# Kernel tuning notes

Hardware: AMD Instinct MI355X
Metric: run time of the kernel (lower is better)

Reference implementation:

```python
import jax, jax.numpy as jnp
import numpy as np

B, S, D, H = 2, 2048, 2048, 16
HD = D // H  # 128


def setup_inputs() -> dict:
    key = jax.random.key(0)
    ks = jax.random.split(key, 5)
    x = jax.random.normal(ks[0], (B, S, D), dtype=jnp.float32)
    scale = 1.0 / np.sqrt(D)
    wq = jax.random.normal(ks[1], (D, D), dtype=jnp.float32) * scale
    wk = jax.random.normal(ks[2], (D, D), dtype=jnp.float32) * scale
    wv = jax.random.normal(ks[3], (D, D), dtype=jnp.float32) * scale
    wo = jax.random.normal(ks[4], (D, D), dtype=jnp.float32) * scale
    # RoPE frequencies: theta = 10000, freqs_cis[t, j] = exp(i * t / theta^(2j/HD))
    inv_freq = 1.0 / (10000.0 ** (jnp.arange(0, HD, 2, dtype=jnp.float32) / HD))  # [HD/2]
    t = jnp.arange(S, dtype=jnp.float32)
    ang = jnp.outer(t, inv_freq)  # [S, HD/2]
    freqs_cos = jnp.cos(ang)
    freqs_sin = jnp.sin(ang)
    # Additive causal mask [S, S]
    neg = jnp.float32(-1e9)
    mask = jnp.triu(jnp.full((S, S), neg, dtype=jnp.float32), k=1)
    return {"x": x, "wq": wq, "wk": wk, "wv": wv, "wo": wo,
            "freqs_cos": freqs_cos, "freqs_sin": freqs_sin,
            "mask": mask, "start_pos": 0}


def _rope(t, cos, sin):
    # t: [B, S, H, HD]; cos/sin: [S, HD/2] broadcast as [1, S, 1, HD/2]
    tr = t.reshape(t.shape[:-1] + (HD // 2, 2))
    xr, xi = tr[..., 0], tr[..., 1]
    c = cos[None, :, None, :]
    s = sin[None, :, None, :]
    out_r = xr * c - xi * s
    out_i = xr * s + xi * c
    return jnp.stack([out_r, out_i], axis=-1).reshape(t.shape)


def reference(x, wq, wk, wv, wo, freqs_cos, freqs_sin, mask, start_pos):
    bsz, seqlen, _ = x.shape
    # nn.Linear: y = x @ W.T
    xq = jnp.einsum('bsd,ed->bse', x, wq).reshape(bsz, seqlen, H, HD)
    xk = jnp.einsum('bsd,ed->bse', x, wk).reshape(bsz, seqlen, H, HD)
    xv = jnp.einsum('bsd,ed->bse', x, wv).reshape(bsz, seqlen, H, HD)
    xq = _rope(xq, freqs_cos, freqs_sin)
    xk = _rope(xk, freqs_cos, freqs_sin)
    # [B, H, S, HD]
    xq = xq.transpose(0, 2, 1, 3)
    xk = xk.transpose(0, 2, 1, 3)
    xv = xv.transpose(0, 2, 1, 3)
    scores = jnp.einsum('bhqd,bhkd->bhqk', xq, xk) / jnp.sqrt(jnp.float32(HD))
    scores = scores + mask[None, None, :, :]
    probs = jax.nn.softmax(scores.astype(jnp.float32), axis=-1).astype(xq.dtype)
    out = jnp.einsum('bhqk,bhkd->bhqd', probs, xv)
    out = out.transpose(0, 2, 1, 3).reshape(bsz, seqlen, H * HD)
    return jnp.einsum('bse,de->bsd', out, wo)
```

## Files before the change

### kernel.cpp

```cpp
#include <hip/hip_runtime.h>


#define SQ 2048
#define DQ 2048
#define HQ 16
#define HDQ 128

typedef short bf16x8 __attribute__((ext_vector_type(8)));
typedef short bf16x4 __attribute__((ext_vector_type(4)));
typedef float f32x4 __attribute__((ext_vector_type(4)));

#define WAITVM4 asm volatile("s_waitcnt vmcnt(4)" ::: "memory")
#define WAITVM3 asm volatile("s_waitcnt vmcnt(3)" ::: "memory")
#define WAITVM2 asm volatile("s_waitcnt vmcnt(2)" ::: "memory")
#define WAITVM0 asm volatile("s_waitcnt vmcnt(0)" ::: "memory")

__device__ __forceinline__ short f2bf(float f) {
  union { float f; unsigned u; } v; v.f = f;
  unsigned r = (v.u + 0x7FFFu + ((v.u >> 16) & 1u)) >> 16;
  return (short)r;
}
__device__ __forceinline__ float bf2f(short b) {
  union { unsigned u; float f; } v; v.u = ((unsigned)(unsigned short)b) << 16;
  return v.f;
}
__device__ __forceinline__ void gload_lds16(const void* g, void* l) {
  __builtin_amdgcn_global_load_lds(
      (const __attribute__((address_space(1))) void*)g,
      (__attribute__((address_space(3))) void*)l, 16, 0, 0);
}

__global__ void cvt5_kernel(const float* __restrict__ x, const float* __restrict__ wq,
                            const float* __restrict__ wk, const float* __restrict__ wv,
                            const float* __restrict__ wo, short* __restrict__ xb,
                            short* __restrict__ wqb, short* __restrict__ wkb,
                            short* __restrict__ wvb, short* __restrict__ wob) {
  int bi = blockIdx.x;
  const float* src;
  short* dst;
  int off;
  if (bi < 4096) {
    src = x; dst = xb; off = bi;
  } else {
    int t = bi - 4096, wsel = t >> 11;
    off = t & 2047;
    src = (wsel == 0) ? wq : (wsel == 1) ? wk : (wsel == 2) ? wv : wo;
    dst = (wsel == 0) ? wqb : (wsel == 1) ? wkb : (wsel == 2) ? wvb : wob;
  }
  int i = off * 256 + threadIdx.x;
  const f32x4* p = (const f32x4*)src + (size_t)i * 2;
  f32x4 a = p[0], b = p[1];
  bf16x8 o;
  o[0] = f2bf(a[0]); o[1] = f2bf(a[1]); o[2] = f2bf(a[2]); o[3] = f2bf(a[3]);
  o[4] = f2bf(b[0]); o[5] = f2bf(b[1]); o[6] = f2bf(b[2]); o[7] = f2bf(b[3]);
  *((bf16x8*)dst + i) = o;
}

__global__ void tpose_kernel(const float* __restrict__ fc, const float* __restrict__ fs,
                             float* __restrict__ fct, float* __restrict__ fst) {
  __shared__ float tile[64][65];
  int s0 = blockIdx.x * 64, t = threadIdx.x;
#pragma unroll
  for (int it = 0; it < 16; ++it) {
    int idx = it * 256 + t;
    int r = idx >> 6, ii = idx & 63;
    tile[r][ii] = fc[(size_t)(s0 + r) * 64 + ii];
  }
  __syncthreads();
#pragma unroll
  for (int it = 0; it < 16; ++it) {
    int idx = it * 256 + t;
    int ii = idx >> 6, so = idx & 63;
    fct[(size_t)ii * 2048 + s0 + so] = tile[so][ii];
  }
  __syncthreads();
#pragma unroll
  for (int it = 0; it < 16; ++it) {
    int idx = it * 256 + t;
    int r = idx >> 6, ii = idx & 63;
    tile[r][ii] = fs[(size_t)(s0 + r) * 64 + ii];
  }
  __syncthreads();
#pragma unroll
  for (int it = 0; it < 16; ++it) {
    int idx = it * 256 + t;
    int ii = idx >> 6, so = idx & 63;
    fst[(size_t)ii * 2048 + s0 + so] = tile[so][ii];
  }
}

template <int BN, int MODE>
__global__ __launch_bounds__(512, 4) void gemmT(const short* __restrict__ A,
                                                const short* __restrict__ W,
                                                short* __restrict__ oQ, short* __restrict__ oK,
                                                short* __restrict__ oV, float* __restrict__ oF,
                                                const float* __restrict__ cosTt,
                                                const float* __restrict__ sinTt) {
  constexpr int NFR = BN / 64;
  constexpr int NIB = BN / 16;
  __shared__ __align__(16) short As[3][128 * 32];
  __shared__ __align__(16) short Bs[3][BN * 32];
  const int K = DQ;
  const int NT = K / 32;
  int x = blockIdx.x, xcd = x & 7, l = x >> 3;
  int by, bx;
  if (MODE == 0) {
    int xr = xcd >> 2, xc = xcd & 3;
    by = xr * 16 + (l >> 3);
    bx = xc * 8 + (l & 7);
  } else {
    int xr = xcd >> 1, xc = xcd & 1;
    by = xr * 8 + (l >> 3);
    bx = xc * 8 + (l & 7);
  }
  int m0 = by * 128, n0 = bx * BN;
  int tid = threadIdx.x, wid = tid >> 6, lane = tid & 63;
  int wr = wid >> 2, wc = wid & 3;
  f32x4 acc[4][NFR] = {};

  auto stageA = [&](int kt, int buf) {
    int g = wid * 64 + lane;
    int r = g >> 2, q = g & 3;
    gload_lds16(A + (size_t)(m0 + r) * K + kt * 32 + ((q ^ (((r >> 3) & 1) << 1)) * 8),
                &As[buf][wid * 512]);
  };
  auto stageB = [&](int kt, int buf) {
#pragma unroll
    for (int i = wid; i < NIB; i += 8) {
      int g = i * 64 + lane;
      int r = g >> 2, q = g & 3;
      gload_lds16(W + (size_t)(n0 + r) * K + kt * 32 + ((q ^ (((r >> 3) & 1) << 1)) * 8),
                  &Bs[buf][i * 512]);
    }
  };

  stageA(0, 0); stageB(0, 0);
  stageA(1, 1); stageB(1, 1);
  if (BN == 192 && wid < 4) { WAITVM3; } else { WAITVM2; }
  __builtin_amdgcn_s_barrier();

  int cc = (lane >> 4) * 8;
  int cur = 0, nbuf = 2;
#pragma unroll 1
  for (int t = 0; t < NT; ++t) {
    bool st = (t + 2) < NT;
    bf16x8 bfr[NFR], af[4];
#pragma unroll
    for (int nf = 0; nf < NFR; ++nf) {
      int br = wc * (BN / 4) + nf * 16 + (lane & 15);
      bfr[nf] = *(const bf16x8*)&Bs[cur][br * 32 + (cc ^ (((br >> 3) & 1) << 4))];
    }
#pragma unroll
    for (int i = 0; i < 4; ++i) {
      int fr = wr * 64 + i * 16 + (lane & 15);
      af[i] = *(const bf16x8*)&As[cur][fr * 32 + (cc ^ (((fr >> 3) & 1) << 4))];
    }
    if (st) { stageA(t + 2, nbuf); stageB(t + 2, nbuf); }
    __builtin_amdgcn_s_setprio(1);
#pragma unroll
    for (int i = 0; i < 4; ++i)
#pragma unroll
      for (int nf = 0; nf < NFR; ++nf)
        acc[i][nf] = __builtin_amdgcn_mfma_f32_16x16x32_bf16(af[i], bfr[nf], acc[i][nf], 0, 0, 0);
    __builtin_amdgcn_s_setprio(0);
    if (st) {
      if (BN == 192 && wid < 4) { WAITVM3; } else { WAITVM2; }
    } else {
      WAITVM0;
    }
    __builtin_amdgcn_s_barrier();
    cur = (cur == 2) ? 0 : cur + 1;
    nbuf = (nbuf == 2) ? 0 : nbuf + 1;
  }
  if (MODE == 1) {
#pragma unroll
    for (int mf = 0; mf < 4; ++mf) {
      int mb = m0 + wr * 64 + mf * 16 + (lane >> 4) * 4;
#pragma unroll
      for (int nf = 0; nf < NFR; ++nf) {
        int n_lin = n0 + wc * (BN / 4) + nf * 16 + (lane & 15);
#pragma unroll
        for (int j = 0; j < 4; ++j)
          oF[(size_t)(mb + j) * DQ + n_lin] = acc[mf][nf][j];
      }
    }
  } else {
#pragma unroll
    for (int nf = 0; nf < NFR; ++nf) {
      int n_lin = n0 + wc * (BN / 4) + nf * 16 + (lane & 15);
      int zsel = n_lin >> 11, col = n_lin & 2047;
      int h = col >> 7, hd = col & 127, ii = hd >> 1;
      if (zsel < 2) {
        float sgn = (hd & 1) ? 1.f : -1.f;
        float scl = (zsel == 0) ? 0.12751744779976827f : 1.f;
        int sb = (m0 & 2047) + wr * 64 + (lane >> 4) * 4;
        f32x4 cv[4], sv[4];
#pragma unroll
        for (int mf = 0; mf < 4; ++mf) {
          cv[mf] = *(const f32x4*)&cosTt[(size_t)ii * 2048 + sb + mf * 16];
          sv[mf] = *(const f32x4*)&sinTt[(size_t)ii * 2048 + sb + mf * 16];
        }
        short* oT = zsel ? oK : oQ;
#pragma unroll
        for (int mf = 0; mf < 4; ++mf) {
          int mb = m0 + wr * 64 + mf * 16 + (lane >> 4) * 4;
#pragma unroll
          for (int j = 0; j < 4; ++j) {
            float v = acc[mf][nf][j];
            float vp = __shfl_xor(v, 1);
            float o = (v * cv[mf][j] + sgn * vp * sv[mf][j]) * scl;
            int m = mb + j;
            int s = m & 2047, bb = m >> 11;
            oT[(((size_t)(bb * HQ + h)) * SQ + s) * HDQ + hd] = f2bf(o);
          }
        }
      } else {
#pragma unroll
        for (int mf = 0; mf < 4; ++mf) {
          int mb = m0 + wr * 64 + mf * 16 + (lane >> 4) * 4;
          int bb = mb >> 11, s = mb & 2047;
          bf16x4 pk;
          pk[0] = f2bf(acc[mf][nf][0]); pk[1] = f2bf(acc[mf][nf][1]);
          pk[2] = f2bf(acc[mf][nf][2]); pk[3] = f2bf(acc[mf][nf][3]);
          *(bf16x4*)&oV[(((size_t)(bb * HQ + h)) * HDQ + hd) * SQ + s] = pk;
        }
      }
      __builtin_amdgcn_sched_barrier(0);
    }
  }
}

__device__ __forceinline__ void stage_kv32(const short* kbase, const short* vbase, int k0,
                                           short* KsB, short* VtB, int w, int lane) {
#pragma unroll
  for (int i = 0; i < 2; ++i) {
    int c = i * 4 + w;
    int ch = c * 64 + lane;
    int r = ch >> 4, c8 = (ch & 15) * 8;
    gload_lds16(kbase + (size_t)(k0 + r) * HDQ + (c8 ^ ((r & 7) << 3)), KsB + c * 512);
    int d = ch >> 2, k8 = (ch & 3) * 8;
    gload_lds16(vbase + (size_t)d * SQ + k0 + (k8 ^ (((d >> 1) & 3) << 3)), VtB + c * 512);
  }
}

__global__ __launch_bounds__(256, 4) void flash_kernel(const short* __restrict__ qb,
                                                       const short* __restrict__ kb,
                                                       const short* __restrict__ vtb,
                                                       short* __restrict__ ab) {
  __shared__ __align__(16) short Ks[2][32 * 128];
  __shared__ __align__(16) short Vt[2][128 * 32];
  __shared__ __align__(16) short Pl[4][16 * 32];
  int x = blockIdx.x, bh = blockIdx.y;
  int qt = (bh & 8) ? (31 - x) : x;
  int q0 = qt * 64;
  int tid = threadIdx.x, w = tid >> 6, lane = tid & 63;
  int g = lane >> 4, qcol = lane & 15;
  int qw0 = q0 + w * 16;
  const short* qbase = qb + (size_t)bh * SQ * HDQ;
  const short* kbase = kb + (size_t)bh * SQ * HDQ;
  const short* vbase = vtb + (size_t)bh * HDQ * SQ;
  int b = bh >> 4, h = bh & 15;

  bf16x8 qf[4];
#pragma unroll
  for (int ccq = 0; ccq < 4; ++ccq)
    qf[ccq] = *(const bf16x8*)&qbase[(size_t)(qw0 + qcol) * HDQ + ccq * 32 + g * 8];

  f32x4 oacc[8] = {};
  float m_st = -1e30f, l_st = 0.f;
  int nt = 2 * qt + 2;
  stage_kv32(kbase, vbase, 0, Ks[0], Vt[0], w, lane);
#pragma unroll 1
  for (int t = 0; t < nt; ++t) {
    int cur = t & 1;
    int k0 = t * 32;
    __builtin_amdgcn_s_barrier();
    if (t + 1 < nt) {
      stage_kv32(kbase, vbase, (t + 1) * 32, Ks[cur ^ 1], Vt[cur ^ 1], w, lane);
      WAITVM4;
    } else {
      WAITVM0;
    }
    __builtin_amdgcn_s_barrier();
    if (k0 > qw0 + 15) continue;
    f32x4 sacc[2] = {};
    __builtin_amdgcn_s_setprio(1);
#pragma unroll
    for (int nf = 0; nf < 2; ++nf) {
      int rk = nf * 16 + qcol;
#pragma unroll
      for (int ccq = 0; ccq < 4; ++ccq) {
        int ck = ccq * 32 + g * 8;
        bf16x8 kf = *(const bf16x8*)&Ks[cur][rk * 128 + (ck ^ ((rk & 7) << 3))];
        sacc[nf] = __builtin_amdgcn_mfma_f32_16x16x32_bf16(kf, qf[ccq], sacc[nf], 0, 0, 0);
      }
    }
    __builtin_amdgcn_s_setprio(0);
    int q = qw0 + qcol;
    if (k0 + 31 > qw0) {
#pragma unroll
      for (int nf = 0; nf < 2; ++nf)
#pragma unroll
        for (int j = 0; j < 4; ++j) {
          int k = k0 + nf * 16 + g * 4 + j;
          if (k > q) sacc[nf][j] = -1e9f;
        }
    }
    float mt = fmaxf(fmaxf(fmaxf(sacc[0][0], sacc[0][1]), fmaxf(sacc[0][2], sacc[0][3])),
                     fmaxf(fmaxf(sacc[1][0], sacc[1][1]), fmaxf(sacc[1][2], sacc[1][3])));
    mt = fmaxf(mt, __shfl_xor(mt, 16));
    mt = fmaxf(mt, __shfl_xor(mt, 32));
    float mn = fmaxf(m_st, mt);
    float al = exp2f(m_st - mn);
    float p0[4], p1[4];
    float ls = 0.f;
#pragma unroll
    for (int j = 0; j < 4; ++j) { p0[j] = exp2f(sacc[0][j] - mn); ls += p0[j]; }
#pragma unroll
    for (int j = 0; j < 4; ++j) { p1[j] = exp2f(sacc[1][j] - mn); ls += p1[j]; }
    l_st = l_st * al + ls;
    m_st = mn;
    int sw = (qcol & 3) * 8;
    {
      bf16x4 pk;
      pk[0] = f2bf(p0[0]); pk[1] = f2bf(p0[1]); pk[2] = f2bf(p0[2]); pk[3] = f2bf(p0[3]);
      *(bf16x4*)&Pl[w][qcol * 32 + ((g * 4) ^ sw)] = pk;
      pk[0] = f2bf(p1[0]); pk[1] = f2bf(p1[1]); pk[2] = f2bf(p1[2]); pk[3] = f2bf(p1[3]);
      *(bf16x4*)&Pl[w][qcol * 32 + ((16 + g * 4) ^ sw)] = pk;
    }
    f32x4 alv;
    alv[0] = __shfl(al, g * 4 + 0);
    alv[1] = __shfl(al, g * 4 + 1);
    alv[2] = __shfl(al, g * 4 + 2);
    alv[3] = __shfl(al, g * 4 + 3);
#pragma unroll
    for (int df = 0; df < 8; ++df) oacc[df] *= alv;
    bf16x8 pf = *(const bf16x8*)&Pl[w][qcol * 32 + ((g * 8) ^ sw)];
    __builtin_amdgcn_s_setprio(1);
#pragma unroll
    for (int df = 0; df < 8; ++df) {
      int rd = df * 16 + qcol;
      bf16x8 vf = *(const bf16x8*)&Vt[cur][rd * 32 + ((g * 8) ^ (((rd >> 1) & 3) << 3))];
      oacc[df] = __builtin_amdgcn_mfma_f32_16x16x32_bf16(pf, vf, oacc[df], 0, 0, 0);
    }
    __builtin_amdgcn_s_setprio(0);
  }
  l_st += __shfl_xor(l_st, 16);
  l_st += __shfl_xor(l_st, 32);
  float inv = 1.0f / l_st;
  f32x4 invv;
  invv[0] = __shfl(inv, g * 4 + 0);
  invv[1] = __shfl(inv, g * 4 + 1);
  invv[2] = __shfl(inv, g * 4 + 2);
  invv[3] = __shfl(inv, g * 4 + 3);
#pragma unroll
  for (int df = 0; df < 8; ++df)
#pragma unroll
    for (int j = 0; j < 4; ++j) {
      int qq = qw0 + g * 4 + j;
      int dd = df * 16 + qcol;
      ab[((size_t)b * SQ + qq) * DQ + h * HDQ + dd] = f2bf(oacc[df][j] * invv[j]);
    }
}

extern "C" void kernel_launch(void* const* d_in, const int* in_sizes, int n_in,
                              void* d_out, int out_size, void* d_ws, size_t ws_size,
                              hipStream_t stream) {
  (void)in_sizes; (void)n_in; (void)out_size; (void)ws_size;
  const float* x  = (const float*)d_in[0];
  const float* wq = (const float*)d_in[1];
  const float* wk = (const float*)d_in[2];
  const float* wv = (const float*)d_in[3];
  const float* wo = (const float*)d_in[4];
  const float* fc = (const float*)d_in[5];
  const float* fs = (const float*)d_in[6];
  float* out = (float*)d_out;

  short* xb  = (short*)d_ws;
  short* wqb = xb + (size_t)8388608;
  short* wkb = wqb + (size_t)4194304;
  short* wvb = wkb + (size_t)4194304;
  short* wob = wvb + (size_t)4194304;
  short* qb  = wob + (size_t)4194304;
  short* kb  = qb + (size_t)8388608;
  short* ab  = kb + (size_t)8388608;
  float* fct = (float*)d_out;
  float* fst = fct + (size_t)131072;
  short* vtb = (short*)d_out + (size_t)8388608;

  cvt5_kernel<<<12288, 256, 0, stream>>>(x, wq, wk, wv, wo, xb, wqb, wkb, wvb, wob);
  tpose_kernel<<<32, 256, 0, stream>>>(fc, fs, fct, fst);

  gemmT<192, 0><<<dim3(1024), 512, 0, stream>>>(xb, wqb, qb, kb, vtb, nullptr, fct, fst);

  flash_kernel<<<dim3(32, 32), 256, 0, stream>>>(qb, kb, vtb, ab);

  gemmT<128, 1><<<dim3(512), 512, 0, stream>>>(ab, wob, nullptr, nullptr, nullptr, out,
                                               nullptr, nullptr);
}
```

Measured before the change: 273.8 us.

## Replace QKV GEMM with 256x256-tile, eight-phase pipelined kernel with RoPE epilogue

The fused QKV projection moves from a 128x192 tile, three-stage, BK=32 GEMM to a dedicated kernel with 256x256 tiles and BK=64. Loads are split into half-tile stages interleaved across eight MFMA phases per iteration, with barriers and prioritised MFMA sections. The aim is more reuse per loaded byte and better overlap of global-to-LDS loads with compute. The grid shrinks to 384 blocks at one block per CU with heavy register and LDS use, which risks an uneven wave on 256 CUs and less latency hiding. The output GEMM is split off as a non-templated copy.

Result: slower. 286.1 us (+4.5%).

```diff
diff --git a/kernel.cpp b/kernel.cpp
--- a/kernel.cpp
+++ b/kernel.cpp
@@ -10,10 +10,11 @@
 typedef short bf16x4 __attribute__((ext_vector_type(4)));
 typedef float f32x4 __attribute__((ext_vector_type(4)));
 
+#define WAITVM6 asm volatile("s_waitcnt vmcnt(6)" ::: "memory")
 #define WAITVM4 asm volatile("s_waitcnt vmcnt(4)" ::: "memory")
-#define WAITVM3 asm volatile("s_waitcnt vmcnt(3)" ::: "memory")
 #define WAITVM2 asm volatile("s_waitcnt vmcnt(2)" ::: "memory")
 #define WAITVM0 asm volatile("s_waitcnt vmcnt(0)" ::: "memory")
+#define BAR __builtin_amdgcn_s_barrier()
 
 __device__ __forceinline__ short f2bf(float f) {
   union { float f; unsigned u; } v; v.f = f;
@@ -89,34 +90,244 @@
   }
 }
 
-template <int BN, int MODE>
-__global__ __launch_bounds__(512, 4) void gemmT(const short* __restrict__ A,
+__global__ __launch_bounds__(512, 1) void qkv8p(const short* __restrict__ A,
                                                 const short* __restrict__ W,
                                                 short* __restrict__ oQ, short* __restrict__ oK,
-                                                short* __restrict__ oV, float* __restrict__ oF,
+                                                short* __restrict__ oV,
                                                 const float* __restrict__ cosTt,
                                                 const float* __restrict__ sinTt) {
-  constexpr int NFR = BN / 64;
-  constexpr int NIB = BN / 16;
+  __shared__ __align__(16) short As[2][2][128 * 64];
+  __shared__ __align__(16) short Bs[2][2][128 * 64];
+  const int K = DQ;
+  const int NT = K / 64;
+  const int NI = NT / 2;
+  int xb_ = blockIdx.x, xcd = xb_ & 7, l = xb_ >> 3;
+  int by = l & 15, bx = xcd * 3 + (l >> 4);
+  int m0 = by * 256, n0 = bx * 256;
+  int tid = threadIdx.x, wid = tid >> 6, lane = tid & 63;
+  int wr = wid >> 2, wc = wid & 3;
+  f32x4 acc[8][4] = {};
+
+  auto stageH = [&](const short* g, short* ldst) {
+#pragma unroll
+    for (int i = 0; i < 2; ++i) {
+      int gg = i * 512 + tid;
+      int r = gg >> 3, q = gg & 7;
+      gload_lds16(g + (size_t)r * K + ((q ^ (r & 7)) * 8), ldst + i * 4096 + wid * 512);
+    }
+  };
+  auto rdA = [&](int buf, int a, int kk) -> bf16x8 {
+    int rl = a * 16 + (lane & 15);
+    int q = kk * 4 + (lane >> 4);
+    return *(const bf16x8*)&As[buf][wr][rl * 64 + ((q ^ (rl & 7)) * 8)];
+  };
+  auto rdB = [&](int buf, int b, int kk) -> bf16x8 {
+    int rl = (wc & 1) * 64 + b * 16 + (lane & 15);
+    int q = kk * 4 + (lane >> 4);
+    return *(const bf16x8*)&Bs[buf][wc >> 1][rl * 64 + ((q ^ (rl & 7)) * 8)];
+  };
+
+  stageH(W + (size_t)n0 * K, &Bs[0][0][0]);
+  stageH(W + (size_t)(n0 + 128) * K, &Bs[0][1][0]);
+  stageH(A + (size_t)m0 * K, &As[0][0][0]);
+  stageH(A + (size_t)(m0 + 128) * K, &As[0][1][0]);
+  stageH(W + (size_t)n0 * K + 64, &Bs[1][0][0]);
+  stageH(W + (size_t)(n0 + 128) * K + 64, &Bs[1][1][0]);
+  stageH(A + (size_t)m0 * K + 64, &As[1][0][0]);
+  WAITVM6;
+  BAR;
+
+  bf16x8 aq[4][2], bp0[2][2], bp1[2][2];
+#pragma unroll 1
+  for (int it = 0; it < NI; ++it) {
+    const bool st = (it < NI - 1);
+    const int t1 = 2 * it + 1, t2 = 2 * it + 2, t3 = 2 * it + 3;
+#pragma unroll
+    for (int b = 0; b < 2; ++b)
+#pragma unroll
+      for (int kk = 0; kk < 2; ++kk) bp0[b][kk] = rdB(0, b, kk);
+#pragma unroll
+    for (int a = 0; a < 4; ++a)
+#pragma unroll
+      for (int kk = 0; kk < 2; ++kk) aq[a][kk] = rdA(0, a, kk);
+    stageH(A + (size_t)(m0 + 128) * K + (size_t)t1 * 64, &As[1][1][0]);
+    BAR;
+    __builtin_amdgcn_s_setprio(1);
+#pragma unroll
+    for (int a = 0; a < 4; ++a)
+#pragma unroll
+      for (int b = 0; b < 2; ++b)
+#pragma unroll
+        for (int kk = 0; kk < 2; ++kk)
+          acc[a][b] = __builtin_amdgcn_mfma_f32_16x16x32_bf16(aq[a][kk], bp0[b][kk], acc[a][b], 0, 0, 0);
+    __builtin_amdgcn_s_setprio(0);
+    BAR;
+#pragma unroll
+    for (int b = 0; b < 2; ++b)
+#pragma unroll
+      for (int kk = 0; kk < 2; ++kk) bp1[b][kk] = rdB(0, 2 + b, kk);
+    BAR;
+    __builtin_amdgcn_s_setprio(1);
+#pragma unroll
+    for (int a = 0; a < 4; ++a)
+#pragma unroll
+      for (int b = 0; b < 2; ++b)
+#pragma unroll
+        for (int kk = 0; kk < 2; ++kk)
+          acc[a][2 + b] = __builtin_amdgcn_mfma_f32_16x16x32_bf16(aq[a][kk], bp1[b][kk], acc[a][2 + b], 0, 0, 0);
+    __builtin_amdgcn_s_setprio(0);
+    BAR;
+#pragma unroll
+    for (int a = 0; a < 4; ++a)
+#pragma unroll
+      for (int kk = 0; kk < 2; ++kk) aq[a][kk] = rdA(0, 4 + a, kk);
+    if (st) stageH(W + (size_t)n0 * K + (size_t)t2 * 64, &Bs[0][0][0]);
+    BAR;
+    __builtin_amdgcn_s_setprio(1);
+#pragma unroll
+    for (int a = 0; a < 4; ++a)
+#pragma unroll
+      for (int b = 0; b < 2; ++b)
+#pragma unroll
+        for (int kk = 0; kk < 2; ++kk)
+          acc[4 + a][2 + b] = __builtin_amdgcn_mfma_f32_16x16x32_bf16(aq[a][kk], bp1[b][kk], acc[4 + a][2 + b], 0, 0, 0);
+    __builtin_amdgcn_s_setprio(0);
+    BAR;
+    if (st) stageH(W + (size_t)(n0 + 128) * K + (size_t)t2 * 64, &Bs[0][1][0]);
+    BAR;
+    __builtin_amdgcn_s_setprio(1);
+#pragma unroll
+    for (int a = 0; a < 4; ++a)
+#pragma unroll
+      for (int b = 0; b < 2; ++b)
+#pragma unroll
+        for (int kk = 0; kk < 2; ++kk)
+          acc[4 + a][b] = __builtin_amdgcn_mfma_f32_16x16x32_bf16(aq[a][kk], bp0[b][kk], acc[4 + a][b], 0, 0, 0);
+    __builtin_amdgcn_s_setprio(0);
+    if (st) { WAITVM4; } else { WAITVM0; }
+    BAR;
+#pragma unroll
+    for (int b = 0; b < 2; ++b)
+#pragma unroll
+      for (int kk = 0; kk < 2; ++kk) bp0[b][kk] = rdB(1, b, kk);
+#pragma unroll
+    for (int a = 0; a < 4; ++a)
+#pragma unroll
+      for (int kk = 0; kk < 2; ++kk) aq[a][kk] = rdA(1, a, kk);
+    if (st) stageH(A + (size_t)m0 * K + (size_t)t2 * 64, &As[0][0][0]);
+    BAR;
+    __builtin_amdgcn_s_setprio(1);
+#pragma unroll
+    for (int a = 0; a < 4; ++a)
+#pragma unroll
+      for (int b = 0; b < 2; ++b)
+#pragma unroll
+        for (int kk = 0; kk < 2; ++kk)
+          acc[a][b] = __builtin_amdgcn_mfma_f32_16x16x32_bf16(aq[a][kk], bp0[b][kk], acc[a][b], 0, 0, 0);
+    __builtin_amdgcn_s_setprio(0);
+    BAR;
+#pragma unroll
+    for (int b = 0; b < 2; ++b)
+#pragma unroll
+      for (int kk = 0; kk < 2; ++kk) bp1[b][kk] = rdB(1, 2 + b, kk);
+    if (st) stageH(A + (size_t)(m0 + 128) * K + (size_t)t2 * 64, &As[0][1][0]);
+    BAR;
+    __builtin_amdgcn_s_setprio(1);
+#pragma unroll
+    for (int a = 0; a < 4; ++a)
+#pragma unroll
+      for (int b = 0; b < 2; ++b)
+#pragma unroll
+        for (int kk = 0; kk < 2; ++kk)
+          acc[a][2 + b] = __builtin_amdgcn_mfma_f32_16x16x32_bf16(aq[a][kk], bp1[b][kk], acc[a][2 + b], 0, 0, 0);
+    __builtin_amdgcn_s_setprio(0);
+    BAR;
+#pragma unroll
+    for (int a = 0; a < 4; ++a)
+#pragma unroll
+      for (int kk = 0; kk < 2; ++kk) aq[a][kk] = rdA(1, 4 + a, kk);
+    if (st) stageH(W + (size_t)n0 * K + (size_t)t3 * 64, &Bs[1][0][0]);
+    BAR;
+    __builtin_amdgcn_s_setprio(1);
+#pragma unroll
+    for (int a = 0; a < 4; ++a)
+#pragma unroll
+      for (int b = 0; b < 2; ++b)
+#pragma unroll
+        for (int kk = 0; kk < 2; ++kk)
+          acc[4 + a][2 + b] = __builtin_amdgcn_mfma_f32_16x16x32_bf16(aq[a][kk], bp1[b][kk], acc[4 + a][2 + b], 0, 0, 0);
+    __builtin_amdgcn_s_setprio(0);
+    BAR;
+    if (st) {
+      stageH(W + (size_t)(n0 + 128) * K + (size_t)t3 * 64, &Bs[1][1][0]);
+      stageH(A + (size_t)m0 * K + (size_t)t3 * 64, &As[1][0][0]);
+    }
+    BAR;
+    __builtin_amdgcn_s_setprio(1);
+#pragma unroll
+    for (int a = 0; a < 4; ++a)
+#pragma unroll
+      for (int b = 0; b < 2; ++b)
+#pragma unroll
+        for (int kk = 0; kk < 2; ++kk)
+          acc[4 + a][b] = __builtin_amdgcn_mfma_f32_16x16x32_bf16(aq[a][kk], bp0[b][kk], acc[4 + a][b], 0, 0, 0);
+    __builtin_amdgcn_s_setprio(0);
+    if (st) { WAITVM6; }
+    BAR;
+  }
+  int bb = m0 >> 11;
+  int sb = (m0 & 2047) + wr * 128 + (lane >> 4) * 4;
+#pragma unroll
+  for (int b = 0; b < 4; ++b) {
+    int n_lin = n0 + wc * 64 + b * 16 + (lane & 15);
+    int zsel = n_lin >> 11, col = n_lin & 2047;
+    int h = col >> 7, hd = col & 127, ii = hd >> 1;
+    if (zsel < 2) {
+      float sgn = (hd & 1) ? 1.f : -1.f;
+      float scl = (zsel == 0) ? 0.12751744779976827f : 1.f;
+      short* oT = zsel ? oK : oQ;
+#pragma unroll
+      for (int a = 0; a < 8; ++a) {
+        f32x4 cvv = *(const f32x4*)&cosTt[(size_t)ii * 2048 + sb + a * 16];
+        f32x4 svv = *(const f32x4*)&sinTt[(size_t)ii * 2048 + sb + a * 16];
+#pragma unroll
+        for (int j = 0; j < 4; ++j) {
+          float v = acc[a][b][j];
+          float vp = __shfl_xor(v, 1);
+          float o = (v * cvv[j] + sgn * vp * svv[j]) * scl;
+          int s = sb + a * 16 + j;
+          oT[(((size_t)(bb * HQ + h)) * SQ + s) * HDQ + hd] = f2bf(o);
+        }
+      }
+    } else {
+#pragma unroll
+      for (int a = 0; a < 8; ++a) {
+        int s = sb + a * 16;
+        bf16x4 pk;
+        pk[0] = f2bf(acc[a][b][0]); pk[1] = f2bf(acc[a][b][1]);
+        pk[2] = f2bf(acc[a][b][2]); pk[3] = f2bf(acc[a][b][3]);
+        *(bf16x4*)&oV[(((size_t)(bb * HQ + h)) * HDQ + hd) * SQ + s] = pk;
+      }
+    }
+    __builtin_amdgcn_sched_barrier(0);
+  }
+}
+
+__global__ __launch_bounds__(512, 4) void gemm_out(const short* __restrict__ A,
+                                                   const short* __restrict__ W,
+                                                   float* __restrict__ oF) {
   __shared__ __align__(16) short As[3][128 * 32];
-  __shared__ __align__(16) short Bs[3][BN * 32];
+  __shared__ __align__(16) short Bs[3][128 * 32];
   const int K = DQ;
   const int NT = K / 32;
   int x = blockIdx.x, xcd = x & 7, l = x >> 3;
-  int by, bx;
-  if (MODE == 0) {
-    int xr = xcd >> 2, xc = xcd & 3;
-    by = xr * 16 + (l >> 3);
-    bx = xc * 8 + (l & 7);
-  } else {
-    int xr = xcd >> 1, xc = xcd & 1;
-    by = xr * 8 + (l >> 3);
-    bx = xc * 8 + (l & 7);
-  }
-  int m0 = by * 128, n0 = bx * BN;
+  int xr = xcd >> 1, xc = xcd & 1;
+  int by = xr * 8 + (l >> 3);
+  int bx = xc * 8 + (l & 7);
+  int m0 = by * 128, n0 = bx * 128;
   int tid = threadIdx.x, wid = tid >> 6, lane = tid & 63;
   int wr = wid >> 2, wc = wid & 3;
-  f32x4 acc[4][NFR] = {};
+  f32x4 acc[4][2] = {};
 
   auto stageA = [&](int kt, int buf) {
     int g = wid * 64 + lane;
@@ -125,18 +336,15 @@
                 &As[buf][wid * 512]);
   };
   auto stageB = [&](int kt, int buf) {
-#pragma unroll
-    for (int i = wid; i < NIB; i += 8) {
-      int g = i * 64 + lane;
-      int r = g >> 2, q = g & 3;
-      gload_lds16(W + (size_t)(n0 + r) * K + kt * 32 + ((q ^ (((r >> 3) & 1) << 1)) * 8),
-                  &Bs[buf][i * 512]);
-    }
+    int g = wid * 64 + lane;
+    int r = g >> 2, q = g & 3;
+    gload_lds16(W + (size_t)(n0 + r) * K + kt * 32 + ((q ^ (((r >> 3) & 1) << 1)) * 8),
+                &Bs[buf][wid * 512]);
   };
 
   stageA(0, 0); stageB(0, 0);
   stageA(1, 1); stageB(1, 1);
-  if (BN == 192 && wid < 4) { WAITVM3; } else { WAITVM2; }
+  WAITVM2;
   __builtin_amdgcn_s_barrier();
 
   int cc = (lane >> 4) * 8;
@@ -144,10 +352,10 @@
 #pragma unroll 1
   for (int t = 0; t < NT; ++t) {
     bool st = (t + 2) < NT;
-    bf16x8 bfr[NFR], af[4];
-#pragma unroll
-    for (int nf = 0; nf < NFR; ++nf) {
-      int br = wc * (BN / 4) + nf * 16 + (lane & 15);
+    bf16x8 bfr[2], af[4];
+#pragma unroll
+    for (int nf = 0; nf < 2; ++nf) {
+      int br = wc * 32 + nf * 16 + (lane & 15);
       bfr[nf] = *(const bf16x8*)&Bs[cur][br * 32 + (cc ^ (((br >> 3) & 1) << 4))];
     }
 #pragma unroll
@@ -160,72 +368,23 @@
 #pragma unroll
     for (int i = 0; i < 4; ++i)
 #pragma unroll
-      for (int nf = 0; nf < NFR; ++nf)
+      for (int nf = 0; nf < 2; ++nf)
         acc[i][nf] = __builtin_amdgcn_mfma_f32_16x16x32_bf16(af[i], bfr[nf], acc[i][nf], 0, 0, 0);
     __builtin_amdgcn_s_setprio(0);
-    if (st) {
-      if (BN == 192 && wid < 4) { WAITVM3; } else { WAITVM2; }
-    } else {
-      WAITVM0;
-    }
+    if (st) { WAITVM2; } else { WAITVM0; }
     __builtin_amdgcn_s_barrier();
     cur = (cur == 2) ? 0 : cur + 1;
     nbuf = (nbuf == 2) ? 0 : nbuf + 1;
   }
-  if (MODE == 1) {
-#pragma unroll
-    for (int mf = 0; mf < 4; ++mf) {
-      int mb = m0 + wr * 64 + mf * 16 + (lane >> 4) * 4;
-#pragma unroll
-      for (int nf = 0; nf < NFR; ++nf) {
-        int n_lin = n0 + wc * (BN / 4) + nf * 16 + (lane & 15);
-#pragma unroll
-        for (int j = 0; j < 4; ++j)
-          oF[(size_t)(mb + j) * DQ + n_lin] = acc[mf][nf][j];
-      }
-    }
-  } else {
-#pragma unroll
-    for (int nf = 0; nf < NFR; ++nf) {
-      int n_lin = n0 + wc * (BN / 4) + nf * 16 + (lane & 15);
-      int zsel = n_lin >> 11, col = n_lin & 2047;
-      int h = col >> 7, hd = col & 127, ii = hd >> 1;
-      if (zsel < 2) {
-        float sgn = (hd & 1) ? 1.f : -1.f;
-        float scl = (zsel == 0) ? 0.12751744779976827f : 1.f;
-        int sb = (m0 & 2047) + wr * 64 + (lane >> 4) * 4;
-        f32x4 cv[4], sv[4];
-#pragma unroll
-        for (int mf = 0; mf < 4; ++mf) {
-          cv[mf] = *(const f32x4*)&cosTt[(size_t)ii * 2048 + sb + mf * 16];
-          sv[mf] = *(const f32x4*)&sinTt[(size_t)ii * 2048 + sb + mf * 16];
-        }
-        short* oT = zsel ? oK : oQ;
-#pragma unroll
-        for (int mf = 0; mf < 4; ++mf) {
-          int mb = m0 + wr * 64 + mf * 16 + (lane >> 4) * 4;
-#pragma unroll
-          for (int j = 0; j < 4; ++j) {
-            float v = acc[mf][nf][j];
-            float vp = __shfl_xor(v, 1);
-            float o = (v * cv[mf][j] + sgn * vp * sv[mf][j]) * scl;
-            int m = mb + j;
-            int s = m & 2047, bb = m >> 11;
-            oT[(((size_t)(bb * HQ + h)) * SQ + s) * HDQ + hd] = f2bf(o);
-          }
-        }
-      } else {
-#pragma unroll
-        for (int mf = 0; mf < 4; ++mf) {
-          int mb = m0 + wr * 64 + mf * 16 + (lane >> 4) * 4;
-          int bb = mb >> 11, s = mb & 2047;
-          bf16x4 pk;
-          pk[0] = f2bf(acc[mf][nf][0]); pk[1] = f2bf(acc[mf][nf][1]);
-          pk[2] = f2bf(acc[mf][nf][2]); pk[3] = f2bf(acc[mf][nf][3]);
-          *(bf16x4*)&oV[(((size_t)(bb * HQ + h)) * HDQ + hd) * SQ + s] = pk;
-        }
-      }
-      __builtin_amdgcn_sched_barrier(0);
+#pragma unroll
+  for (int mf = 0; mf < 4; ++mf) {
+    int mb = m0 + wr * 64 + mf * 16 + (lane >> 4) * 4;
+#pragma unroll
+    for (int nf = 0; nf < 2; ++nf) {
+      int n_lin = n0 + wc * 32 + nf * 16 + (lane & 15);
+#pragma unroll
+      for (int j = 0; j < 4; ++j)
+        oF[(size_t)(mb + j) * DQ + n_lin] = acc[mf][nf][j];
     }
   }
 }
@@ -391,10 +550,9 @@
   cvt5_kernel<<<12288, 256, 0, stream>>>(x, wq, wk, wv, wo, xb, wqb, wkb, wvb, wob);
   tpose_kernel<<<32, 256, 0, stream>>>(fc, fs, fct, fst);
 
-  gemmT<192, 0><<<dim3(1024), 512, 0, stream>>>(xb, wqb, qb, kb, vtb, nullptr, fct, fst);
+  qkv8p<<<dim3(384), 512, 0, stream>>>(xb, wqb, qb, kb, vtb, fct, fst);
 
   flash_kernel<<<dim3(32, 32), 256, 0, stream>>>(qb, kb, vtb, ab);
 
-  gemmT<128, 1><<<dim3(512), 512, 0, stream>>>(ab, wob, nullptr, nullptr, nullptr, out,
-                                               nullptr, nullptr);
-}
+  gemm_out<<<dim3(512), 512, 0, stream>>>(ab, wob, out);
+}
```
